# Kernel optimization log

Hardware: AMD Instinct MI355X
Metric: run time of the kernel (lower is better)

The kernel has to match this reference:

```python
import jax, jax.numpy as jnp
import numpy as np

N_NODES = 40000
N_EDGES = 640000
BATCH = 2
IN_DIM = 3
HID = 128
OUT_DIM = 3


def setup_inputs() -> dict:
    key = jax.random.key(0)
    ks = jax.random.split(key, 16)
    p = jax.random.normal(ks[0], (BATCH, N_NODES, IN_DIM), dtype=jnp.float32)
    edge_rows = jax.random.randint(ks[1], (N_EDGES,), 0, N_NODES, dtype=jnp.int32)
    edge_cols = jax.random.randint(ks[2], (N_EDGES,), 0, N_NODES, dtype=jnp.int32)
    # normalize_sparse_matrix: divide each nonzero (value 1.0) by the row's nonzero count
    deg = jax.ops.segment_sum(jnp.ones((N_EDGES,), jnp.float32), edge_rows, num_segments=N_NODES)
    adj_vals = 1.0 / deg[edge_rows]  # every used row has deg >= 1
    s = 0.05
    # initial Linear(3 -> 128)
    W_init = jax.random.normal(ks[3], (IN_DIM, HID), jnp.float32) * s
    b_init = jnp.zeros((HID,), jnp.float32)
    # 4 GraphConvs inside the two blocks (all 128->128), each has filter + self_filter
    Wf_blocks = jax.random.normal(ks[4], (4, HID, HID), jnp.float32) * s
    bf_blocks = jnp.zeros((4, HID), jnp.float32)
    Ws_blocks = jax.random.normal(ks[5], (4, HID, HID), jnp.float32) * s
    bs_blocks = jnp.zeros((4, HID), jnp.float32)
    # final GraphConvLayer (128 -> 3)
    Wf_out = jax.random.normal(ks[6], (HID, OUT_DIM), jnp.float32) * s
    bf_out = jnp.zeros((OUT_DIM,), jnp.float32)
    Ws_out = jax.random.normal(ks[7], (HID, OUT_DIM), jnp.float32) * s
    bs_out = jnp.zeros((OUT_DIM,), jnp.float32)
    return dict(p=p, adj_vals=adj_vals, edge_rows=edge_rows, edge_cols=edge_cols,
                W_init=W_init, b_init=b_init,
                Wf_blocks=Wf_blocks, bf_blocks=bf_blocks,
                Ws_blocks=Ws_blocks, bs_blocks=bs_blocks,
                Wf_out=Wf_out, bf_out=bf_out, Ws_out=Ws_out, bs_out=bs_out)


def reference(p, adj_vals, edge_rows, edge_cols,
              W_init, b_init,
              Wf_blocks, bf_blocks, Ws_blocks, bs_blocks,
              Wf_out, bf_out, Ws_out, bs_out):
    n = p.shape[1]

    def spmm(xb):  # xb: [N, d] -> A @ xb via edge-list scatter-add
        return jax.ops.segment_sum(adj_vals[:, None] * xb[edge_cols], edge_rows, num_segments=n)

    spmm_b = jax.vmap(spmm)  # [B, N, d]

    def gconv(x, Wf, bf, Ws, bs):
        # sparse path: self_filter(x) + filter(spmm(adj, x))
        return (x @ Ws + bs) + (spmm_b(x) @ Wf + bf)

    x = p @ W_init + b_init  # [B, N, HID]
    for blk in range(2):  # two GraphConvBlocks, residual, no shortcut (dims equal)
        net = gconv(jax.nn.relu(x), Wf_blocks[2 * blk], bf_blocks[2 * blk],
                    Ws_blocks[2 * blk], bs_blocks[2 * blk])
        dx = gconv(jax.nn.relu(net), Wf_blocks[2 * blk + 1], bf_blocks[2 * blk + 1],
                   Ws_blocks[2 * blk + 1], bs_blocks[2 * blk + 1])
        x = x + dx
    # final GraphConvLayer 128 -> 3
    out = gconv(jax.nn.relu(x), Wf_out, bf_out, Ws_out, bs_out)
    return out
```

## Files before the change

kernel.cpp:

```cpp
#include <hip/hip_runtime.h>


typedef unsigned short u16;
typedef unsigned int   u32;
typedef __bf16 bf8_t __attribute__((ext_vector_type(8)));
typedef float  f4_t  __attribute__((ext_vector_type(4)));

#define N_NODES 40000
#define N_EDGES 640000
#define BN      80000

__device__ __forceinline__ float bf2f(u16 u) {
  union { u32 i; float f; } v; v.i = ((u32)u) << 16; return v.f;
}
__device__ __forceinline__ u16 f2bf(float f) {
  union { float f; u32 i; } v; v.f = f;
  u32 i = v.i;
  return (u16)((i + 0x7FFFu + ((i >> 16) & 1u)) >> 16);
}
__device__ __forceinline__ float asf(u32 i) {
  union { u32 u; float f; } v; v.u = i; return v.f;
}
__device__ __forceinline__ u32 pack2(float a, float b) {
  return (u32)f2bf(a) | ((u32)f2bf(b) << 16);
}
__device__ __forceinline__ float lo2f(u32 v) { return asf(v << 16); }
__device__ __forceinline__ float hi2f(u32 v) { return asf(v & 0xffff0000u); }
__device__ __forceinline__ u32 relu2(u32 v) {
  u32 r = v;
  if (r & 0x8000u)     r &= 0xffff0000u;
  if (r & 0x80000000u) r &= 0x0000ffffu;
  return r;
}

__global__ void fill_kernel(float* __restrict__ out, int n, float v) {
  int i = blockIdx.x * 256 + threadIdx.x;
  if (i < n) out[i] = v;
}

__global__ void hist_kernel(const int* __restrict__ rows, int* __restrict__ cnt) {
  int e = blockIdx.x * 256 + threadIdx.x;
  if (e < N_EDGES) atomicAdd(&cnt[rows[e]], 1);
}

__global__ void scan1_kernel(const int* __restrict__ cnt, int* __restrict__ row_ptr,
                             int* __restrict__ blocksum) {
  __shared__ int sm[256];
  int t = threadIdx.x;
  int row = blockIdx.x * 256 + t;
  int v = (row < N_NODES) ? cnt[row] : 0;
  sm[t] = v; __syncthreads();
  for (int off = 1; off < 256; off <<= 1) {
    int u = (t >= off) ? sm[t - off] : 0;
    __syncthreads();
    sm[t] += u;
    __syncthreads();
  }
  if (row < N_NODES) row_ptr[row] = sm[t] - v;
  if (t == 255) blocksum[blockIdx.x] = sm[255];
}

__global__ void scan2_kernel(int* __restrict__ blocksum, int* __restrict__ row_ptr, int nblk) {
  __shared__ int sm[256];
  int t = threadIdx.x;
  int v = (t < nblk) ? blocksum[t] : 0;
  sm[t] = v; __syncthreads();
  for (int off = 1; off < 256; off <<= 1) {
    int u = (t >= off) ? sm[t - off] : 0;
    __syncthreads();
    sm[t] += u;
    __syncthreads();
  }
  if (t < nblk) blocksum[t] = sm[t] - v;
  if (t == 255) row_ptr[N_NODES] = sm[255];
}

__global__ void scan3_kernel(int* __restrict__ row_ptr, const int* __restrict__ blocksum,
                             int* __restrict__ cnt) {
  int row = blockIdx.x * 256 + threadIdx.x;
  if (row < N_NODES) {
    int rp = row_ptr[row] + blocksum[blockIdx.x];
    row_ptr[row] = rp;
    cnt[row] = rp;
  }
}

__global__ void scatter_kernel(const int* __restrict__ rows, const int* __restrict__ cols,
                               int* __restrict__ cur, int* __restrict__ cols_s) {
  int e = blockIdx.x * 256 + threadIdx.x;
  if (e < N_EDGES) {
    int r = rows[e];
    int pos = atomicAdd(&cur[r], 1);
    cols_s[pos] = cols[e];
  }
}

__global__ void wprep_kernel(const float* __restrict__ Wf_b, const float* __restrict__ Ws_b,
                             const float* __restrict__ bf_b, const float* __restrict__ bs_b,
                             u16* __restrict__ WtCat, float* __restrict__ biasCat) {
  int idx = blockIdx.x * 256 + threadIdx.x;
  int g = idx >> 15, rem = idx & 32767;
  int h = rem >> 8, k = rem & 255;
  float v = (k < 128) ? Ws_b[(g * 128 + k) * 128 + h]
                      : Wf_b[(g * 128 + (k - 128)) * 128 + h];
  WtCat[idx] = f2bf(v);
  if (k == 0) biasCat[g * 128 + h] = bs_b[g * 128 + h] + bf_b[g * 128 + h];
}

__global__ void init_kernel(const float* __restrict__ p, const float* __restrict__ W,
                            const float* __restrict__ bias, u16* __restrict__ xb,
                            u16* __restrict__ rA) {
  int idx = blockIdx.x * 256 + threadIdx.x;
  int row = idx >> 6;
  int h = (idx & 63) * 2;
  float p0 = p[row * 3], p1 = p[row * 3 + 1], p2 = p[row * 3 + 2];
  float s0 = p0 * W[h]     + p1 * W[128 + h]     + p2 * W[256 + h]     + bias[h];
  float s1 = p0 * W[h + 1] + p1 * W[128 + h + 1] + p2 * W[256 + h + 1] + bias[h + 1];
  size_t o = (size_t)row * 64 + (h >> 1);
  ((u32*)xb)[o] = pack2(s0, s1);
  ((u32*)rA)[o] = pack2(s0 > 0.f ? s0 : 0.f, s1 > 0.f ? s1 : 0.f);
}

#define ACC8(u, a0, a1, a2, a3, a4, a5, a6, a7)                           \
  a0 += asf((u).x << 16); a1 += asf((u).x & 0xffff0000u);                 \
  a2 += asf((u).y << 16); a3 += asf((u).y & 0xffff0000u);                 \
  a4 += asf((u).z << 16); a5 += asf((u).z & 0xffff0000u);                 \
  a6 += asf((u).w << 16); a7 += asf((u).w & 0xffff0000u);

__global__ void spmm_kernel(const int* __restrict__ row_ptr, const int* __restrict__ cols_s,
                            const u16* __restrict__ xin, u16* __restrict__ yout) {
  int row = blockIdx.x * 4 + (threadIdx.x >> 6);
  int l = threadIdx.x & 63;
  int g = l >> 4, sl = l & 15;
  int s = row_ptr[row], e = row_ptr[row + 1];
  const uint4* X0 = (const uint4*)xin + sl;
  const uint4* X1 = X0 + 640000;
  float a0 = 0.f, a1 = 0.f, a2 = 0.f, a3 = 0.f, a4 = 0.f, a5 = 0.f, a6 = 0.f, a7 = 0.f;
  float b0 = 0.f, b1 = 0.f, b2 = 0.f, b3 = 0.f, b4 = 0.f, b5 = 0.f, b6 = 0.f, b7 = 0.f;
  int i = s;
  for (; i + 7 < e; i += 8) {
    int c0 = cols_s[i + g], c1 = cols_s[i + 4 + g];
    uint4 u00 = X0[(size_t)c0 * 16];
    uint4 u01 = X1[(size_t)c0 * 16];
    uint4 u10 = X0[(size_t)c1 * 16];
    uint4 u11 = X1[(size_t)c1 * 16];
    ACC8(u00, a0, a1, a2, a3, a4, a5, a6, a7);
    ACC8(u01, b0, b1, b2, b3, b4, b5, b6, b7);
    ACC8(u10, a0, a1, a2, a3, a4, a5, a6, a7);
    ACC8(u11, b0, b1, b2, b3, b4, b5, b6, b7);
  }
  for (; i + 3 < e; i += 4) {
    int c = cols_s[i + g];
    uint4 u0 = X0[(size_t)c * 16];
    uint4 u1 = X1[(size_t)c * 16];
    ACC8(u0, a0, a1, a2, a3, a4, a5, a6, a7);
    ACC8(u1, b0, b1, b2, b3, b4, b5, b6, b7);
  }
  if (i + g < e) {
    int c = cols_s[i + g];
    uint4 u0 = X0[(size_t)c * 16];
    uint4 u1 = X1[(size_t)c * 16];
    ACC8(u0, a0, a1, a2, a3, a4, a5, a6, a7);
    ACC8(u1, b0, b1, b2, b3, b4, b5, b6, b7);
  }
  a0 += __shfl_xor(a0, 16); a1 += __shfl_xor(a1, 16); a2 += __shfl_xor(a2, 16); a3 += __shfl_xor(a3, 16);
  a4 += __shfl_xor(a4, 16); a5 += __shfl_xor(a5, 16); a6 += __shfl_xor(a6, 16); a7 += __shfl_xor(a7, 16);
  b0 += __shfl_xor(b0, 16); b1 += __shfl_xor(b1, 16); b2 += __shfl_xor(b2, 16); b3 += __shfl_xor(b3, 16);
  b4 += __shfl_xor(b4, 16); b5 += __shfl_xor(b5, 16); b6 += __shfl_xor(b6, 16); b7 += __shfl_xor(b7, 16);
  a0 += __shfl_xor(a0, 32); a1 += __shfl_xor(a1, 32); a2 += __shfl_xor(a2, 32); a3 += __shfl_xor(a3, 32);
  a4 += __shfl_xor(a4, 32); a5 += __shfl_xor(a5, 32); a6 += __shfl_xor(a6, 32); a7 += __shfl_xor(a7, 32);
  b0 += __shfl_xor(b0, 32); b1 += __shfl_xor(b1, 32); b2 += __shfl_xor(b2, 32); b3 += __shfl_xor(b3, 32);
  b4 += __shfl_xor(b4, 32); b5 += __shfl_xor(b5, 32); b6 += __shfl_xor(b6, 32); b7 += __shfl_xor(b7, 32);
  float sc = (e > s) ? 1.f / (float)(e - s) : 0.f;
  if (g == 0) {
    uint4 o;
    o.x = pack2(a0 * sc, a1 * sc);
    o.y = pack2(a2 * sc, a3 * sc);
    o.z = pack2(a4 * sc, a5 * sc);
    o.w = pack2(a6 * sc, a7 * sc);
    *((uint4*)yout + (size_t)row * 16 + sl) = o;
  } else if (g == 1) {
    uint4 o;
    o.x = pack2(b0 * sc, b1 * sc);
    o.y = pack2(b2 * sc, b3 * sc);
    o.z = pack2(b4 * sc, b5 * sc);
    o.w = pack2(b6 * sc, b7 * sc);
    *((uint4*)yout + 640000 + (size_t)row * 16 + sl) = o;
  }
}

#define TS 136
template <int MODE>
__global__ __launch_bounds__(256, 4) void gemm_kernel(
    const u16* __restrict__ rin, const u16* __restrict__ yin,
    const u16* __restrict__ WtCat, const float* __restrict__ biasCat, int g,
    u16* __restrict__ rout, u16* __restrict__ xresid) {
  __shared__ __align__(16) u16 lds[18432];
  u16* ldsA = lds;
  u16* ldsW = lds + 9216;
  int tid = threadIdx.x;
  int m0 = blockIdx.x * 128;
  int li = tid & 15, q = (tid >> 4) & 3, wv = tid >> 6;
  int wmo = (wv >> 1) * 64, wno = (wv & 1) * 64;

  f4_t acc[4][4];
#pragma unroll
  for (int i = 0; i < 4; ++i)
#pragma unroll
    for (int j = 0; j < 4; ++j) acc[i][j] = (f4_t){0.f, 0.f, 0.f, 0.f};

  const u16* Wsrc = WtCat + (size_t)g * 32768;

  for (int kb = 0; kb < 256; kb += 64) {
    __syncthreads();
    const u16* srcA = (kb < 128) ? (rin + kb) : (yin + (kb - 128));
#pragma unroll
    for (int p2 = 0; p2 < 4; ++p2) {
      int idx = p2 * 256 + tid;
      int row = idx >> 3, seg = idx & 7;
      uint4 va = *reinterpret_cast<const uint4*>(srcA + (size_t)(m0 + row) * 128 + seg * 8);
      *reinterpret_cast<uint4*>(&ldsA[row * 72 + seg * 8]) = va;
      uint4 vw = *reinterpret_cast<const uint4*>(Wsrc + (size_t)row * 256 + kb + seg * 8);
      *reinterpret_cast<uint4*>(&ldsW[row * 72 + seg * 8]) = vw;
    }
    __syncthreads();
#pragma unroll
    for (int kk = 0; kk < 64; kk += 32) {
      bf8_t af[4], wf[4];
#pragma unroll
      for (int t = 0; t < 4; ++t)
        af[t] = __builtin_bit_cast(bf8_t,
            *reinterpret_cast<const uint4*>(&ldsA[(wmo + t * 16 + li) * 72 + kk + q * 8]));
#pragma unroll
      for (int t = 0; t < 4; ++t)
        wf[t] = __builtin_bit_cast(bf8_t,
            *reinterpret_cast<const uint4*>(&ldsW[(wno + t * 16 + li) * 72 + kk + q * 8]));
#pragma unroll
      for (int i = 0; i < 4; ++i)
#pragma unroll
        for (int j = 0; j < 4; ++j)
          acc[i][j] = __builtin_amdgcn_mfma_f32_16x16x32_bf16(af[i], wf[j], acc[i][j], 0, 0, 0);
    }
  }

  float bias[4];
#pragma unroll
  for (int j = 0; j < 4; ++j) bias[j] = biasCat[g * 128 + wno + j * 16 + li];

  __syncthreads();
#pragma unroll
  for (int i = 0; i < 4; ++i)
#pragma unroll
    for (int j = 0; j < 4; ++j)
#pragma unroll
      for (int r2 = 0; r2 < 4; ++r2) {
        int m = wmo + i * 16 + q * 4 + r2;
        int col = wno + j * 16 + li;
        lds[m * TS + col] = f2bf(acc[i][j][r2] + bias[j]);
      }
  __syncthreads();

#pragma unroll
  for (int p2 = 0; p2 < 8; ++p2) {
    int idx = p2 * 256 + tid;
    int row = idx >> 4, ch = idx & 15;
    uint4 cv = *reinterpret_cast<const uint4*>(&lds[row * TS + ch * 8]);
    size_t gid = (size_t)(m0 + row) * 16 + ch;
    if (MODE == 0) {
      uint4 o;
      o.x = relu2(cv.x); o.y = relu2(cv.y); o.z = relu2(cv.z); o.w = relu2(cv.w);
      ((uint4*)rout)[gid] = o;
    } else {
      uint4 xv = ((const uint4*)xresid)[gid];
      uint4 nx, nr;
      float x0, x1;
      x0 = lo2f(xv.x) + lo2f(cv.x); x1 = hi2f(xv.x) + hi2f(cv.x);
      nx.x = pack2(x0, x1); nr.x = pack2(x0 > 0.f ? x0 : 0.f, x1 > 0.f ? x1 : 0.f);
      x0 = lo2f(xv.y) + lo2f(cv.y); x1 = hi2f(xv.y) + hi2f(cv.y);
      nx.y = pack2(x0, x1); nr.y = pack2(x0 > 0.f ? x0 : 0.f, x1 > 0.f ? x1 : 0.f);
      x0 = lo2f(xv.z) + lo2f(cv.z); x1 = hi2f(xv.z) + hi2f(cv.z);
      nx.z = pack2(x0, x1); nr.z = pack2(x0 > 0.f ? x0 : 0.f, x1 > 0.f ? x1 : 0.f);
      x0 = lo2f(xv.w) + lo2f(cv.w); x1 = hi2f(xv.w) + hi2f(cv.w);
      nx.w = pack2(x0, x1); nr.w = pack2(x0 > 0.f ? x0 : 0.f, x1 > 0.f ? x1 : 0.f);
      ((uint4*)xresid)[gid] = nx;
      ((uint4*)rout)[gid] = nr;
    }
  }
}

__global__ void zproj_kernel(const u16* __restrict__ rA,
                             const float* __restrict__ Wfo, const float* __restrict__ Wso,
                             const float* __restrict__ bfo, const float* __restrict__ bso,
                             float4* __restrict__ zf4, float4* __restrict__ zs4) {
  int row = blockIdx.x * 4 + (threadIdx.x >> 6);
  int l = threadIdx.x & 63;
  u32 ra = ((const u32*)rA)[(size_t)row * 64 + l];
  float r0 = asf(ra << 16), r1 = asf(ra & 0xffff0000u);
  int ch = l * 2;
  float f0 = r0 * Wfo[ch * 3 + 0] + r1 * Wfo[ch * 3 + 3];
  float f1 = r0 * Wfo[ch * 3 + 1] + r1 * Wfo[ch * 3 + 4];
  float f2 = r0 * Wfo[ch * 3 + 2] + r1 * Wfo[ch * 3 + 5];
  float s0 = r0 * Wso[ch * 3 + 0] + r1 * Wso[ch * 3 + 3];
  float s1 = r0 * Wso[ch * 3 + 1] + r1 * Wso[ch * 3 + 4];
  float s2 = r0 * Wso[ch * 3 + 2] + r1 * Wso[ch * 3 + 5];
#pragma unroll
  for (int off = 32; off >= 1; off >>= 1) {
    f0 += __shfl_down(f0, off); f1 += __shfl_down(f1, off); f2 += __shfl_down(f2, off);
    s0 += __shfl_down(s0, off); s1 += __shfl_down(s1, off); s2 += __shfl_down(s2, off);
  }
  if (l == 0) {
    zf4[row] = make_float4(f0, f1, f2, 0.f);
    zs4[row] = make_float4(s0 + bso[0] + bfo[0], s1 + bso[1] + bfo[1], s2 + bso[2] + bfo[2], 0.f);
  }
}

__global__ void spmm3_kernel(const int* __restrict__ row_ptr, const int* __restrict__ cols_s,
                             const float4* __restrict__ zf4, const float4* __restrict__ zs4,
                             float* __restrict__ out) {
  int idx = blockIdx.x * 256 + threadIdx.x;
  if (idx >= BN) return;
  int b = (idx >= N_NODES) ? 1 : 0;
  int r = idx - b * N_NODES;
  int s = row_ptr[r], e = row_ptr[r + 1];
  const float4* Z = zf4 + (size_t)b * N_NODES;
  float a0 = 0.f, a1 = 0.f, a2 = 0.f;
  for (int i = s; i < e; ++i) {
    float4 z = Z[cols_s[i]];
    a0 += z.x; a1 += z.y; a2 += z.z;
  }
  float sc = (e > s) ? 1.f / (float)(e - s) : 0.f;
  float4 zs = zs4[idx];
  out[idx * 3 + 0] = zs.x + a0 * sc;
  out[idx * 3 + 1] = zs.y + a1 * sc;
  out[idx * 3 + 2] = zs.z + a2 * sc;
}

extern "C" void kernel_launch(void* const* d_in, const int* in_sizes, int n_in,
                              void* d_out, int out_size, void* d_ws, size_t ws_size,
                              hipStream_t stream) {
  float* out = (float*)d_out;
  int fill_grid = (out_size + 255) / 256;

  const int exp_sizes[14] = {240000, 640000, 640000, 640000, 384, 128,
                             65536, 512, 65536, 512, 384, 3, 384, 3};
  bool sizes_ok = (n_in == 14);
  if (sizes_ok) for (int i = 0; i < 14; ++i) if (in_sizes[i] != exp_sizes[i]) sizes_ok = false;
  if (!sizes_ok) {
    fill_kernel<<<fill_grid, 256, 0, stream>>>(out, out_size, 1.0f);
    return;
  }

  const size_t NEED = (size_t)4 * BN * 128 * 2 + (size_t)N_EDGES * 4 + 160016 + 160000 + 1024 + 262144 + 2048;
  if (ws_size < NEED) {
    fill_kernel<<<fill_grid, 256, 0, stream>>>(out, out_size, 0.0f);
    return;
  }

  const float* p      = (const float*)d_in[0];
  const int*   erows  = (const int*)d_in[2];
  const int*   ecols  = (const int*)d_in[3];
  const float* W_init = (const float*)d_in[4];
  const float* b_init = (const float*)d_in[5];
  const float* Wf_b   = (const float*)d_in[6];
  const float* bf_b   = (const float*)d_in[7];
  const float* Ws_b   = (const float*)d_in[8];
  const float* bs_b   = (const float*)d_in[9];
  const float* Wf_o   = (const float*)d_in[10];
  const float* bf_o   = (const float*)d_in[11];
  const float* Ws_o   = (const float*)d_in[12];
  const float* bs_o   = (const float*)d_in[13];

  char* w = (char*)d_ws;
  u16*   rA       = (u16*)w;   w += (size_t)BN * 128 * 2;
  u16*   rB       = (u16*)w;   w += (size_t)BN * 128 * 2;
  u16*   y        = (u16*)w;   w += (size_t)BN * 128 * 2;
  u16*   xb       = (u16*)w;   w += (size_t)BN * 128 * 2;
  int*   cols_s   = (int*)w;   w += (size_t)N_EDGES * 4;
  int*   row_ptr  = (int*)w;   w += 160016;
  int*   cnt      = (int*)w;   w += 160000;
  int*   blocksum = (int*)w;   w += 1024;
  u16*   WtCat    = (u16*)w;   w += 4 * 128 * 256 * 2;
  float* biasCat  = (float*)w; w += 4 * 128 * 4;

  float4* zf4 = (float4*)y;
  float4* zs4 = (float4*)(y + 640000);

  const int NBLK = (N_NODES + 255) / 256;

  hipMemsetAsync(cnt, 0, N_NODES * 4, stream);
  hist_kernel<<<2500, 256, 0, stream>>>(erows, cnt);
  scan1_kernel<<<NBLK, 256, 0, stream>>>(cnt, row_ptr, blocksum);
  scan2_kernel<<<1, 256, 0, stream>>>(blocksum, row_ptr, NBLK);
  scan3_kernel<<<NBLK, 256, 0, stream>>>(row_ptr, blocksum, cnt);
  scatter_kernel<<<2500, 256, 0, stream>>>(erows, ecols, cnt, cols_s);
  wprep_kernel<<<512, 256, 0, stream>>>(Wf_b, Ws_b, bf_b, bs_b, WtCat, biasCat);
  init_kernel<<<20000, 256, 0, stream>>>(p, W_init, b_init, xb, rA);

  for (int blk = 0; blk < 2; ++blk) {
    spmm_kernel<<<10000, 256, 0, stream>>>(row_ptr, cols_s, rA, y);
    gemm_kernel<0><<<625, 256, 0, stream>>>(rA, y, WtCat, biasCat, 2 * blk, rB, nullptr);
    spmm_kernel<<<10000, 256, 0, stream>>>(row_ptr, cols_s, rB, y);
    gemm_kernel<1><<<625, 256, 0, stream>>>(rB, y, WtCat, biasCat, 2 * blk + 1, rA, xb);
  }
  zproj_kernel<<<20000, 256, 0, stream>>>(rA, Wf_o, Ws_o, bf_o, bs_o, zf4, zs4);
  spmm3_kernel<<<(BN + 255) / 256, 256, 0, stream>>>(row_ptr, cols_s, zf4, zs4, out);
}
```

Baseline: 456.9 us.

## Fuse relu into spmm/gemm loads, fold zproj into last gemm, merge init kernels

Removes the separate relu(x) buffer: the first spmm of each block applies ReLU on the fly to the residual x, and the first gemm applies ReLU while staging x into LDS. The final block's second gemm computes the 128->3 projections directly in its epilogue, so the separate zproj pass and its re-read of the activations go away. Weight prep and the initial linear layer are merged into one launch. This cuts a full activation write and read per block and two launches, at the cost of extra ALU work in the spmm inner loop and more registers in the gemm epilogue.

```diff
diff --git a/kernel.cpp b/kernel.cpp
--- a/kernel.cpp
+++ b/kernel.cpp
@@ -95,38 +95,31 @@
   }
 }
 
-__global__ void wprep_kernel(const float* __restrict__ Wf_b, const float* __restrict__ Ws_b,
+__global__ void initw_kernel(const float* __restrict__ p, const float* __restrict__ W,
+                             const float* __restrict__ bias, u16* __restrict__ xb,
+                             const float* __restrict__ Wf_b, const float* __restrict__ Ws_b,
                              const float* __restrict__ bf_b, const float* __restrict__ bs_b,
                              u16* __restrict__ WtCat, float* __restrict__ biasCat) {
-  int idx = blockIdx.x * 256 + threadIdx.x;
-  int g = idx >> 15, rem = idx & 32767;
-  int h = rem >> 8, k = rem & 255;
-  float v = (k < 128) ? Ws_b[(g * 128 + k) * 128 + h]
-                      : Wf_b[(g * 128 + (k - 128)) * 128 + h];
-  WtCat[idx] = f2bf(v);
-  if (k == 0) biasCat[g * 128 + h] = bs_b[g * 128 + h] + bf_b[g * 128 + h];
-}
-
-__global__ void init_kernel(const float* __restrict__ p, const float* __restrict__ W,
-                            const float* __restrict__ bias, u16* __restrict__ xb,
-                            u16* __restrict__ rA) {
+  if (blockIdx.x >= 20000) {
+    int idx = (blockIdx.x - 20000) * 256 + threadIdx.x;
+    int g = idx >> 15, rem = idx & 32767;
+    int h = rem >> 8, k = rem & 255;
+    float v = (k < 128) ? Ws_b[(g * 128 + k) * 128 + h]
+                        : Wf_b[(g * 128 + (k - 128)) * 128 + h];
+    WtCat[idx] = f2bf(v);
+    if (k == 0) biasCat[g * 128 + h] = bs_b[g * 128 + h] + bf_b[g * 128 + h];
+    return;
+  }
   int idx = blockIdx.x * 256 + threadIdx.x;
   int row = idx >> 6;
   int h = (idx & 63) * 2;
   float p0 = p[row * 3], p1 = p[row * 3 + 1], p2 = p[row * 3 + 2];
   float s0 = p0 * W[h]     + p1 * W[128 + h]     + p2 * W[256 + h]     + bias[h];
   float s1 = p0 * W[h + 1] + p1 * W[128 + h + 1] + p2 * W[256 + h + 1] + bias[h + 1];
-  size_t o = (size_t)row * 64 + (h >> 1);
-  ((u32*)xb)[o] = pack2(s0, s1);
-  ((u32*)rA)[o] = pack2(s0 > 0.f ? s0 : 0.f, s1 > 0.f ? s1 : 0.f);
-}
-
-#define ACC8(u, a0, a1, a2, a3, a4, a5, a6, a7)                           \
-  a0 += asf((u).x << 16); a1 += asf((u).x & 0xffff0000u);                 \
-  a2 += asf((u).y << 16); a3 += asf((u).y & 0xffff0000u);                 \
-  a4 += asf((u).z << 16); a5 += asf((u).z & 0xffff0000u);                 \
-  a6 += asf((u).w << 16); a7 += asf((u).w & 0xffff0000u);
-
+  ((u32*)xb)[(size_t)row * 64 + (h >> 1)] = pack2(s0, s1);
+}
+
+template <int RELU>
 __global__ void spmm_kernel(const int* __restrict__ row_ptr, const int* __restrict__ cols_s,
                             const u16* __restrict__ xin, u16* __restrict__ yout) {
   int row = blockIdx.x * 4 + (threadIdx.x >> 6);
@@ -135,8 +128,17 @@
   int s = row_ptr[row], e = row_ptr[row + 1];
   const uint4* X0 = (const uint4*)xin + sl;
   const uint4* X1 = X0 + 640000;
-  float a0 = 0.f, a1 = 0.f, a2 = 0.f, a3 = 0.f, a4 = 0.f, a5 = 0.f, a6 = 0.f, a7 = 0.f;
-  float b0 = 0.f, b1 = 0.f, b2 = 0.f, b3 = 0.f, b4 = 0.f, b5 = 0.f, b6 = 0.f, b7 = 0.f;
+  float a[8] = {0.f, 0.f, 0.f, 0.f, 0.f, 0.f, 0.f, 0.f};
+  float b[8] = {0.f, 0.f, 0.f, 0.f, 0.f, 0.f, 0.f, 0.f};
+  auto accum = [&](uint4 u, float* A) {
+#pragma unroll
+    for (int q2 = 0; q2 < 4; ++q2) {
+      u32 v = ((const u32*)&u)[q2];
+      float f0 = lo2f(v), f1 = hi2f(v);
+      if (RELU) { f0 = fmaxf(f0, 0.f); f1 = fmaxf(f1, 0.f); }
+      A[2 * q2] += f0; A[2 * q2 + 1] += f1;
+    }
+  };
   int i = s;
   for (; i + 7 < e; i += 8) {
     int c0 = cols_s[i + g], c1 = cols_s[i + 4 + g];
@@ -144,47 +146,39 @@
     uint4 u01 = X1[(size_t)c0 * 16];
     uint4 u10 = X0[(size_t)c1 * 16];
     uint4 u11 = X1[(size_t)c1 * 16];
-    ACC8(u00, a0, a1, a2, a3, a4, a5, a6, a7);
-    ACC8(u01, b0, b1, b2, b3, b4, b5, b6, b7);
-    ACC8(u10, a0, a1, a2, a3, a4, a5, a6, a7);
-    ACC8(u11, b0, b1, b2, b3, b4, b5, b6, b7);
+    accum(u00, a); accum(u01, b); accum(u10, a); accum(u11, b);
   }
   for (; i + 3 < e; i += 4) {
     int c = cols_s[i + g];
     uint4 u0 = X0[(size_t)c * 16];
     uint4 u1 = X1[(size_t)c * 16];
-    ACC8(u0, a0, a1, a2, a3, a4, a5, a6, a7);
-    ACC8(u1, b0, b1, b2, b3, b4, b5, b6, b7);
+    accum(u0, a); accum(u1, b);
   }
   if (i + g < e) {
     int c = cols_s[i + g];
     uint4 u0 = X0[(size_t)c * 16];
     uint4 u1 = X1[(size_t)c * 16];
-    ACC8(u0, a0, a1, a2, a3, a4, a5, a6, a7);
-    ACC8(u1, b0, b1, b2, b3, b4, b5, b6, b7);
-  }
-  a0 += __shfl_xor(a0, 16); a1 += __shfl_xor(a1, 16); a2 += __shfl_xor(a2, 16); a3 += __shfl_xor(a3, 16);
-  a4 += __shfl_xor(a4, 16); a5 += __shfl_xor(a5, 16); a6 += __shfl_xor(a6, 16); a7 += __shfl_xor(a7, 16);
-  b0 += __shfl_xor(b0, 16); b1 += __shfl_xor(b1, 16); b2 += __shfl_xor(b2, 16); b3 += __shfl_xor(b3, 16);
-  b4 += __shfl_xor(b4, 16); b5 += __shfl_xor(b5, 16); b6 += __shfl_xor(b6, 16); b7 += __shfl_xor(b7, 16);
-  a0 += __shfl_xor(a0, 32); a1 += __shfl_xor(a1, 32); a2 += __shfl_xor(a2, 32); a3 += __shfl_xor(a3, 32);
-  a4 += __shfl_xor(a4, 32); a5 += __shfl_xor(a5, 32); a6 += __shfl_xor(a6, 32); a7 += __shfl_xor(a7, 32);
-  b0 += __shfl_xor(b0, 32); b1 += __shfl_xor(b1, 32); b2 += __shfl_xor(b2, 32); b3 += __shfl_xor(b3, 32);
-  b4 += __shfl_xor(b4, 32); b5 += __shfl_xor(b5, 32); b6 += __shfl_xor(b6, 32); b7 += __shfl_xor(b7, 32);
+    accum(u0, a); accum(u1, b);
+  }
+#pragma unroll
+  for (int k = 0; k < 8; ++k) {
+    a[k] += __shfl_xor(a[k], 16); b[k] += __shfl_xor(b[k], 16);
+    a[k] += __shfl_xor(a[k], 32); b[k] += __shfl_xor(b[k], 32);
+  }
   float sc = (e > s) ? 1.f / (float)(e - s) : 0.f;
   if (g == 0) {
     uint4 o;
-    o.x = pack2(a0 * sc, a1 * sc);
-    o.y = pack2(a2 * sc, a3 * sc);
-    o.z = pack2(a4 * sc, a5 * sc);
-    o.w = pack2(a6 * sc, a7 * sc);
+    o.x = pack2(a[0] * sc, a[1] * sc);
+    o.y = pack2(a[2] * sc, a[3] * sc);
+    o.z = pack2(a[4] * sc, a[5] * sc);
+    o.w = pack2(a[6] * sc, a[7] * sc);
     *((uint4*)yout + (size_t)row * 16 + sl) = o;
   } else if (g == 1) {
     uint4 o;
-    o.x = pack2(b0 * sc, b1 * sc);
-    o.y = pack2(b2 * sc, b3 * sc);
-    o.z = pack2(b4 * sc, b5 * sc);
-    o.w = pack2(b6 * sc, b7 * sc);
+    o.x = pack2(b[0] * sc, b[1] * sc);
+    o.y = pack2(b[2] * sc, b[3] * sc);
+    o.z = pack2(b[4] * sc, b[5] * sc);
+    o.w = pack2(b[6] * sc, b[7] * sc);
     *((uint4*)yout + 640000 + (size_t)row * 16 + sl) = o;
   }
 }
@@ -194,7 +188,10 @@
 __global__ __launch_bounds__(256, 4) void gemm_kernel(
     const u16* __restrict__ rin, const u16* __restrict__ yin,
     const u16* __restrict__ WtCat, const float* __restrict__ biasCat, int g,
-    u16* __restrict__ rout, u16* __restrict__ xresid) {
+    u16* __restrict__ rout, u16* __restrict__ xresid,
+    float4* __restrict__ zf4, float4* __restrict__ zs4,
+    const float* __restrict__ Wfo, const float* __restrict__ Wso,
+    const float* __restrict__ bfo, const float* __restrict__ bso) {
   __shared__ __align__(16) u16 lds[18432];
   u16* ldsA = lds;
   u16* ldsW = lds + 9216;
@@ -219,6 +216,9 @@
       int idx = p2 * 256 + tid;
       int row = idx >> 3, seg = idx & 7;
       uint4 va = *reinterpret_cast<const uint4*>(srcA + (size_t)(m0 + row) * 128 + seg * 8);
+      if (MODE == 0 && kb < 128) {
+        va.x = relu2(va.x); va.y = relu2(va.y); va.z = relu2(va.z); va.w = relu2(va.w);
+      }
       *reinterpret_cast<uint4*>(&ldsA[row * 72 + seg * 8]) = va;
       uint4 vw = *reinterpret_cast<const uint4*>(Wsrc + (size_t)row * 256 + kb + seg * 8);
       *reinterpret_cast<uint4*>(&ldsW[row * 72 + seg * 8]) = vw;
@@ -259,6 +259,18 @@
         lds[m * TS + col] = f2bf(acc[i][j][r2] + bias[j]);
       }
   __syncthreads();
+
+  float wzf[8][3], wzs[8][3];
+  if (MODE == 2) {
+    int chb = (tid & 15) * 8;
+#pragma unroll
+    for (int c = 0; c < 8; ++c)
+#pragma unroll
+      for (int d = 0; d < 3; ++d) {
+        wzf[c][d] = Wfo[(chb + c) * 3 + d];
+        wzs[c][d] = Wso[(chb + c) * 3 + d];
+      }
+  }
 
 #pragma unroll
   for (int p2 = 0; p2 < 8; ++p2) {
@@ -270,47 +282,43 @@
       uint4 o;
       o.x = relu2(cv.x); o.y = relu2(cv.y); o.z = relu2(cv.z); o.w = relu2(cv.w);
       ((uint4*)rout)[gid] = o;
+    } else if (MODE == 1) {
+      uint4 xv = ((const uint4*)xresid)[gid];
+      uint4 nx;
+      float x0, x1;
+      x0 = lo2f(xv.x) + lo2f(cv.x); x1 = hi2f(xv.x) + hi2f(cv.x); nx.x = pack2(x0, x1);
+      x0 = lo2f(xv.y) + lo2f(cv.y); x1 = hi2f(xv.y) + hi2f(cv.y); nx.y = pack2(x0, x1);
+      x0 = lo2f(xv.z) + lo2f(cv.z); x1 = hi2f(xv.z) + hi2f(cv.z); nx.z = pack2(x0, x1);
+      x0 = lo2f(xv.w) + lo2f(cv.w); x1 = hi2f(xv.w) + hi2f(cv.w); nx.w = pack2(x0, x1);
+      ((uint4*)xresid)[gid] = nx;
     } else {
       uint4 xv = ((const uint4*)xresid)[gid];
-      uint4 nx, nr;
-      float x0, x1;
-      x0 = lo2f(xv.x) + lo2f(cv.x); x1 = hi2f(xv.x) + hi2f(cv.x);
-      nx.x = pack2(x0, x1); nr.x = pack2(x0 > 0.f ? x0 : 0.f, x1 > 0.f ? x1 : 0.f);
-      x0 = lo2f(xv.y) + lo2f(cv.y); x1 = hi2f(xv.y) + hi2f(cv.y);
-      nx.y = pack2(x0, x1); nr.y = pack2(x0 > 0.f ? x0 : 0.f, x1 > 0.f ? x1 : 0.f);
-      x0 = lo2f(xv.z) + lo2f(cv.z); x1 = hi2f(xv.z) + hi2f(cv.z);
-      nx.z = pack2(x0, x1); nr.z = pack2(x0 > 0.f ? x0 : 0.f, x1 > 0.f ? x1 : 0.f);
-      x0 = lo2f(xv.w) + lo2f(cv.w); x1 = hi2f(xv.w) + hi2f(cv.w);
-      nx.w = pack2(x0, x1); nr.w = pack2(x0 > 0.f ? x0 : 0.f, x1 > 0.f ? x1 : 0.f);
-      ((uint4*)xresid)[gid] = nx;
-      ((uint4*)rout)[gid] = nr;
+      float zf0 = 0.f, zf1 = 0.f, zf2 = 0.f, zs0 = 0.f, zs1 = 0.f, zs2 = 0.f;
+#pragma unroll
+      for (int q2 = 0; q2 < 4; ++q2) {
+        u32 xu = ((const u32*)&xv)[q2], cu = ((const u32*)&cv)[q2];
+        float r0 = fmaxf(lo2f(xu) + lo2f(cu), 0.f);
+        float r1 = fmaxf(hi2f(xu) + hi2f(cu), 0.f);
+        int c = 2 * q2;
+        zf0 += r0 * wzf[c][0] + r1 * wzf[c + 1][0];
+        zf1 += r0 * wzf[c][1] + r1 * wzf[c + 1][1];
+        zf2 += r0 * wzf[c][2] + r1 * wzf[c + 1][2];
+        zs0 += r0 * wzs[c][0] + r1 * wzs[c + 1][0];
+        zs1 += r0 * wzs[c][1] + r1 * wzs[c + 1][1];
+        zs2 += r0 * wzs[c][2] + r1 * wzs[c + 1][2];
+      }
+#pragma unroll
+      for (int off = 1; off < 16; off <<= 1) {
+        zf0 += __shfl_xor(zf0, off); zf1 += __shfl_xor(zf1, off); zf2 += __shfl_xor(zf2, off);
+        zs0 += __shfl_xor(zs0, off); zs1 += __shfl_xor(zs1, off); zs2 += __shfl_xor(zs2, off);
+      }
+      if ((tid & 15) == 0) {
+        int m = m0 + row;
+        zf4[m] = make_float4(zf0, zf1, zf2, 0.f);
+        zs4[m] = make_float4(zs0 + bso[0] + bfo[0], zs1 + bso[1] + bfo[1],
+                             zs2 + bso[2] + bfo[2], 0.f);
+      }
     }
-  }
-}
-
-__global__ void zproj_kernel(const u16* __restrict__ rA,
-                             const float* __restrict__ Wfo, const float* __restrict__ Wso,
-                             const float* __restrict__ bfo, const float* __restrict__ bso,
-                             float4* __restrict__ zf4, float4* __restrict__ zs4) {
-  int row = blockIdx.x * 4 + (threadIdx.x >> 6);
-  int l = threadIdx.x & 63;
-  u32 ra = ((const u32*)rA)[(size_t)row * 64 + l];
-  float r0 = asf(ra << 16), r1 = asf(ra & 0xffff0000u);
-  int ch = l * 2;
-  float f0 = r0 * Wfo[ch * 3 + 0] + r1 * Wfo[ch * 3 + 3];
-  float f1 = r0 * Wfo[ch * 3 + 1] + r1 * Wfo[ch * 3 + 4];
-  float f2 = r0 * Wfo[ch * 3 + 2] + r1 * Wfo[ch * 3 + 5];
-  float s0 = r0 * Wso[ch * 3 + 0] + r1 * Wso[ch * 3 + 3];
-  float s1 = r0 * Wso[ch * 3 + 1] + r1 * Wso[ch * 3 + 4];
-  float s2 = r0 * Wso[ch * 3 + 2] + r1 * Wso[ch * 3 + 5];
-#pragma unroll
-  for (int off = 32; off >= 1; off >>= 1) {
-    f0 += __shfl_down(f0, off); f1 += __shfl_down(f1, off); f2 += __shfl_down(f2, off);
-    s0 += __shfl_down(s0, off); s1 += __shfl_down(s1, off); s2 += __shfl_down(s2, off);
-  }
-  if (l == 0) {
-    zf4[row] = make_float4(f0, f1, f2, 0.f);
-    zs4[row] = make_float4(s0 + bso[0] + bfo[0], s1 + bso[1] + bfo[1], s2 + bso[2] + bfo[2], 0.f);
   }
 }
 
@@ -371,7 +379,7 @@
   const float* bs_o   = (const float*)d_in[13];
 
   char* w = (char*)d_ws;
-  u16*   rA       = (u16*)w;   w += (size_t)BN * 128 * 2;
+  char*  zbuf     = w;         w += (size_t)BN * 128 * 2;
   u16*   rB       = (u16*)w;   w += (size_t)BN * 128 * 2;
   u16*   y        = (u16*)w;   w += (size_t)BN * 128 * 2;
   u16*   xb       = (u16*)w;   w += (size_t)BN * 128 * 2;
@@ -382,8 +390,8 @@
   u16*   WtCat    = (u16*)w;   w += 4 * 128 * 256 * 2;
   float* biasCat  = (float*)w; w += 4 * 128 * 4;
 
-  float4* zf4 = (float4*)y;
-  float4* zs4 = (float4*)(y + 640000);
+  float4* zf4 = (float4*)zbuf;
+  float4* zs4 = (float4*)(zbuf + 1280000);
 
   const int NBLK = (N_NODES + 255) / 256;
 
@@ -393,15 +401,20 @@
   scan2_kernel<<<1, 256, 0, stream>>>(blocksum, row_ptr, NBLK);
   scan3_kernel<<<NBLK, 256, 0, stream>>>(row_ptr, blocksum, cnt);
   scatter_kernel<<<2500, 256, 0, stream>>>(erows, ecols, cnt, cols_s);
-  wprep_kernel<<<512, 256, 0, stream>>>(Wf_b, Ws_b, bf_b, bs_b, WtCat, biasCat);
-  init_kernel<<<20000, 256, 0, stream>>>(p, W_init, b_init, xb, rA);
+  initw_kernel<<<20512, 256, 0, stream>>>(p, W_init, b_init, xb,
+                                          Wf_b, Ws_b, bf_b, bs_b, WtCat, biasCat);
 
   for (int blk = 0; blk < 2; ++blk) {
-    spmm_kernel<<<10000, 256, 0, stream>>>(row_ptr, cols_s, rA, y);
-    gemm_kernel<0><<<625, 256, 0, stream>>>(rA, y, WtCat, biasCat, 2 * blk, rB, nullptr);
-    spmm_kernel<<<10000, 256, 0, stream>>>(row_ptr, cols_s, rB, y);
-    gemm_kernel<1><<<625, 256, 0, stream>>>(rB, y, WtCat, biasCat, 2 * blk + 1, rA, xb);
-  }
-  zproj_kernel<<<20000, 256, 0, stream>>>(rA, Wf_o, Ws_o, bf_o, bs_o, zf4, zs4);
+    spmm_kernel<1><<<10000, 256, 0, stream>>>(row_ptr, cols_s, xb, y);
+    gemm_kernel<0><<<625, 256, 0, stream>>>(xb, y, WtCat, biasCat, 2 * blk, rB, nullptr,
+                                            nullptr, nullptr, nullptr, nullptr, nullptr, nullptr);
+    spmm_kernel<0><<<10000, 256, 0, stream>>>(row_ptr, cols_s, rB, y);
+    if (blk == 0)
+      gemm_kernel<1><<<625, 256, 0, stream>>>(rB, y, WtCat, biasCat, 1, nullptr, xb,
+                                              nullptr, nullptr, nullptr, nullptr, nullptr, nullptr);
+    else
+      gemm_kernel<2><<<625, 256, 0, stream>>>(rB, y, WtCat, biasCat, 3, nullptr, xb,
+                                              zf4, zs4, Wf_o, Ws_o, bf_o, bs_o);
+  }
   spmm3_kernel<<<(BN + 255) / 256, 256, 0, stream>>>(row_ptr, cols_s, zf4, zs4, out);
 }
```

New measurement: 429.6 us. 1.06x faster.
